# Optimization experiments

Measured on AMD Instinct MI355X. Metric: run time of the kernel, lower is better.

The kernel has to match this reference:

```python
import jax, jax.numpy as jnp
import numpy as np


def setup_inputs() -> dict:
    key = jax.random.key(0)
    k = jax.random.split(key, 5)
    B, S, D, H = 4, 2048, 2048, 8192
    scale1 = 1.0 / np.sqrt(D)
    scale2 = 1.0 / np.sqrt(H)
    return {
        "x": jax.random.normal(k[0], (B, S, D), dtype=jnp.float32),
        "w1": jax.random.normal(k[1], (H, D), dtype=jnp.float32) * scale1,
        "b1": jax.random.normal(k[2], (H,), dtype=jnp.float32) * scale1,
        "w2": jax.random.normal(k[3], (D, H), dtype=jnp.float32) * scale2,
        "b2": jax.random.normal(k[4], (D,), dtype=jnp.float32) * scale2,
    }


def reference(x, w1, b1, w2, b2):
    # fc1: [B,S,D] @ [D,H] -> [B,S,H]
    h = jnp.einsum("bsd,hd->bsh", x, w1) + b1
    # squared ReLU activation
    a = jnp.square(jax.nn.relu(h))
    # fc2: [B,S,H] @ [H,D] -> [B,S,D]
    return jnp.einsum("bsh,dh->bsd", a, w2) + b2
```

## Files before the change

### kernel.cpp

```cpp
#include <hip/hip_runtime.h>
#include <hip/hip_bf16.h>
#include <stdint.h>

typedef __bf16 bf16x8 __attribute__((ext_vector_type(8)));
typedef float f32x4 __attribute__((ext_vector_type(4)));


__device__ inline void gload_lds16(const void* g, void* lds) {
  __builtin_amdgcn_global_load_lds(
      (const __attribute__((address_space(1))) uint32_t*)(uintptr_t)g,
      (__attribute__((address_space(3))) uint32_t*)(uintptr_t)lds,
      16, 0, 0);
}

__device__ inline bf16x8 ds_readv(uint32_t addr) {
  bf16x8 r;
  asm volatile("ds_read_b128 %0, %1" : "=v"(r) : "v"(addr));
  return r;
}

#define LGKM(N) do {                                             \
    asm volatile("s_waitcnt lgkmcnt(" #N ")" ::: "memory");      \
    __builtin_amdgcn_sched_barrier(0);                           \
  } while (0)
#define VM(N) do {                                               \
    asm volatile("s_waitcnt vmcnt(" #N ")" ::: "memory");        \
    __builtin_amdgcn_sched_barrier(0);                           \
  } while (0)

__device__ inline short f2bf(float f) {
  union { float f; uint32_t u; } x; x.f = f;
  uint32_t u = x.u;
  u += 0x7fffu + ((u >> 16) & 1u);
  return (short)(u >> 16);
}

#define BAR() do { asm volatile("" ::: "memory"); \
                   __builtin_amdgcn_s_barrier();  \
                   asm volatile("" ::: "memory"); } while (0)


__global__ __launch_bounds__(256) void cvt_f32_bf16(
    const float* __restrict__ in, short* __restrict__ out, int n4) {
  int i = blockIdx.x * 256 + threadIdx.x;
  if (i < n4) {
    float4 v = reinterpret_cast<const float4*>(in)[i];
    short4 o;
    o.x = f2bf(v.x); o.y = f2bf(v.y); o.z = f2bf(v.z); o.w = f2bf(v.w);
    reinterpret_cast<short4*>(out)[i] = o;
  }
}


template <int EPI>
__global__ __launch_bounds__(512, 2) void gemm_bt(
    const short* __restrict__ A, const short* __restrict__ B,
    const float* __restrict__ bias, void* __restrict__ Cout,
    int M, int N, int K) {
  __shared__ __align__(16) short lds[2][4][128 * 64];

  const int tid  = threadIdx.x;
  const int wave = tid >> 6;
  const int lane = tid & 63;
  const int wr = wave >> 2;
  const int wc = wave & 3;
  const int fr = lane & 15, kq = lane >> 4;

  const int nwg = gridDim.x;
  const int w = (blockIdx.x & 7) * (nwg >> 3) + (blockIdx.x >> 3);
  const int gy = M >> 8;
  const int brow = w % gy;
  const int bcol = w / gy;

  f32x4 acc[8][4];
#pragma unroll
  for (int m = 0; m < 8; ++m)
#pragma unroll
    for (int n = 0; n < 4; ++n)
      acc[m][n] = (f32x4){0.f, 0.f, 0.f, 0.f};

  const int nk = K >> 6;

  const uint32_t LB = (uint32_t)(uintptr_t)&lds[0][0][0];
  uint32_t aA[4][2], aB[2][2];
#pragma unroll
  for (int m = 0; m < 4; ++m)
#pragma unroll
    for (int kk = 0; kk < 2; ++kk) {
      int r = wr * 64 + m * 16 + fr;
      int g = r * 8 + kk * 4 + kq;
      aA[m][kk] = LB + (uint32_t)((g ^ (r & 7)) * 16);
    }
#pragma unroll
  for (int n = 0; n < 2; ++n)
#pragma unroll
    for (int kk = 0; kk < 2; ++kk) {
      int r = wc * 32 + n * 16 + fr;
      int g = r * 8 + kk * 4 + kq;
      aB[n][kk] = LB + (uint32_t)((g ^ (r & 7)) * 16);
    }

  const int i0 = tid;
  const int gl0 = i0 ^ ((i0 >> 3) & 7);
  const int r0 = gl0 >> 3, c0 = gl0 & 7;
  const size_t rstep = (size_t)128 * K;

  const short* pA[2];
  const short* pB[2];
  {
    const int rb0 = (r0 >> 5) * 64 + (r0 & 31);
#pragma unroll
    for (int h = 0; h < 2; ++h) {
      pA[h] = A + (size_t)(brow * 256 + h * 64 + r0) * K + c0 * 8;
      pB[h] = B + (size_t)(bcol * 256 + rb0 + h * 32) * K + c0 * 8;
    }
  }

  const int dst0 = wave * 512, dst1 = 4096 + wave * 512;

#define STAGE(p, buf, slot)                              \
  do {                                                   \
    short* base_ = &lds[buf][slot][0];                   \
    gload_lds16((p), base_ + dst0);                      \
    gload_lds16((p) + rstep, base_ + dst1);              \
    (p) += 64;                                           \
  } while (0)

  bf16x8 a0q[4][2], a1q[4][2], bq0[2][2], bq1[2][2];
  auto Q1 = [&]() {
#pragma unroll
    for (int m = 0; m < 4; ++m)
#pragma unroll
      for (int n = 0; n < 2; ++n)
#pragma unroll
        for (int kk = 0; kk < 2; ++kk)
          acc[m][n] = __builtin_amdgcn_mfma_f32_16x16x32_bf16(
              bq0[n][kk], a0q[m][kk], acc[m][n], 0, 0, 0);
  };
  auto Q2 = [&]() {
#pragma unroll
    for (int m = 0; m < 4; ++m)
#pragma unroll
      for (int n = 0; n < 2; ++n)
#pragma unroll
        for (int kk = 0; kk < 2; ++kk)
          acc[m][n + 2] = __builtin_amdgcn_mfma_f32_16x16x32_bf16(
              bq1[n][kk], a0q[m][kk], acc[m][n + 2], 0, 0, 0);
  };
  auto Q3 = [&]() {
#pragma unroll
    for (int m = 0; m < 4; ++m)
#pragma unroll
      for (int n = 0; n < 2; ++n)
#pragma unroll
        for (int kk = 0; kk < 2; ++kk)
          acc[m + 4][n + 2] = __builtin_amdgcn_mfma_f32_16x16x32_bf16(
              bq1[n][kk], a1q[m][kk], acc[m + 4][n + 2], 0, 0, 0);
  };
  auto Q4 = [&]() {
#pragma unroll
    for (int m = 0; m < 4; ++m)
#pragma unroll
      for (int n = 0; n < 2; ++n)
#pragma unroll
        for (int kk = 0; kk < 2; ++kk)
          acc[m + 4][n] = __builtin_amdgcn_mfma_f32_16x16x32_bf16(
              bq0[n][kk], a1q[m][kk], acc[m + 4][n], 0, 0, 0);
  };
  auto RD_A0 = [&](uint32_t cb) {
#pragma unroll
    for (int m = 0; m < 4; ++m)
#pragma unroll
      for (int kk = 0; kk < 2; ++kk)
        a0q[m][kk] = ds_readv(aA[m][kk] + cb);
  };
  auto RD_A1 = [&](uint32_t cb) {
#pragma unroll
    for (int m = 0; m < 4; ++m)
#pragma unroll
      for (int kk = 0; kk < 2; ++kk)
        a1q[m][kk] = ds_readv(aA[m][kk] + cb + 16384u);
  };
  auto RD_B0 = [&](uint32_t cb) {
#pragma unroll
    for (int n = 0; n < 2; ++n)
#pragma unroll
      for (int kk = 0; kk < 2; ++kk)
        bq0[n][kk] = ds_readv(aB[n][kk] + cb + 32768u);
  };
  auto RD_B1 = [&](uint32_t cb) {
#pragma unroll
    for (int n = 0; n < 2; ++n)
#pragma unroll
      for (int kk = 0; kk < 2; ++kk)
        bq1[n][kk] = ds_readv(aB[n][kk] + cb + 49152u);
  };

#define PRIO_ON  __builtin_amdgcn_s_setprio(1)
#define PRIO_OFF __builtin_amdgcn_s_setprio(0)

  STAGE(pA[0], 0, 0);
  STAGE(pB[0], 0, 2);
  STAGE(pB[1], 0, 3);
  STAGE(pA[1], 0, 1);
  STAGE(pA[0], 1, 0);
  STAGE(pB[0], 1, 2);
  STAGE(pB[1], 1, 3);
  VM(6);
  BAR();

  const int niter = nk >> 1;
  for (int i = 0; i < niter - 1; ++i) {
    RD_A0(0); RD_B0(0);
    STAGE(pA[1], 1, 1);
    LGKM(8);
    BAR();
    LGKM(0);
    PRIO_ON; Q1(); PRIO_OFF;
    VM(10); BAR();
    RD_B1(0);
    STAGE(pA[0], 0, 0);
    BAR();
    LGKM(0);
    PRIO_ON; Q2(); PRIO_OFF;
    VM(10); BAR();
    RD_A1(0);
    STAGE(pB[0], 0, 2);
    BAR();
    LGKM(0);
    PRIO_ON; Q3(); PRIO_OFF;
    VM(10); BAR();
    STAGE(pB[1], 0, 3);
    BAR();
    PRIO_ON; Q4(); PRIO_OFF;
    VM(10); BAR();

    RD_A0(65536u); RD_B0(65536u);
    STAGE(pA[1], 0, 1);
    LGKM(8);
    BAR();
    LGKM(0);
    PRIO_ON; Q1(); PRIO_OFF;
    VM(10); BAR();
    RD_B1(65536u);
    STAGE(pA[0], 1, 0);
    BAR();
    LGKM(0);
    PRIO_ON; Q2(); PRIO_OFF;
    VM(10); BAR();
    RD_A1(65536u);
    STAGE(pB[0], 1, 2);
    BAR();
    LGKM(0);
    PRIO_ON; Q3(); PRIO_OFF;
    VM(10); BAR();
    STAGE(pB[1], 1, 3);
    BAR();
    PRIO_ON; Q4(); PRIO_OFF;
    VM(10); BAR();
  }

  RD_A0(0); RD_B0(0);
  STAGE(pA[1], 1, 1);
  LGKM(8);
  BAR();
  LGKM(0);
  PRIO_ON; Q1(); PRIO_OFF;
  VM(0); BAR();
  RD_B1(0); BAR(); LGKM(0);
  PRIO_ON; Q2(); PRIO_OFF; BAR();
  RD_A1(0); BAR(); LGKM(0);
  PRIO_ON; Q3(); PRIO_OFF; BAR();
  PRIO_ON; Q4(); PRIO_OFF;
  BAR();
  RD_A0(65536u); RD_B0(65536u); BAR(); LGKM(0);
  PRIO_ON; Q1(); PRIO_OFF; BAR();
  RD_B1(65536u); BAR(); LGKM(0);
  PRIO_ON; Q2(); PRIO_OFF; BAR();
  RD_A1(65536u); BAR(); LGKM(0);
  PRIO_ON; Q3(); PRIO_OFF; BAR();
  PRIO_ON; Q4(); PRIO_OFF;

  const int q = lane >> 4;
  if (EPI == 0) {
    short* C = (short*)Cout;
#pragma unroll
    for (int m = 0; m < 8; ++m) {
      const int row = brow * 256 + wr * 128 + m * 16 + fr;
#pragma unroll
      for (int n = 0; n < 4; ++n) {
        const int col = bcol * 256 + wc * 64 + n * 16 + q * 4;
        const float4 bv = *(const float4*)&bias[col];
        short4 o;
        float v0 = acc[m][n][0] + bv.x; v0 = v0 > 0.f ? v0 * v0 : 0.f;
        float v1 = acc[m][n][1] + bv.y; v1 = v1 > 0.f ? v1 * v1 : 0.f;
        float v2 = acc[m][n][2] + bv.z; v2 = v2 > 0.f ? v2 * v2 : 0.f;
        float v3 = acc[m][n][3] + bv.w; v3 = v3 > 0.f ? v3 * v3 : 0.f;
        o.x = f2bf(v0); o.y = f2bf(v1); o.z = f2bf(v2); o.w = f2bf(v3);
        *(short4*)&C[(size_t)row * N + col] = o;
      }
    }
  } else {
    float* C = (float*)Cout;
#pragma unroll
    for (int m = 0; m < 8; ++m) {
      const int row = brow * 256 + wr * 128 + m * 16 + fr;
#pragma unroll
      for (int n = 0; n < 4; ++n) {
        const int col = bcol * 256 + wc * 64 + n * 16 + q * 4;
        const float4 bv = *(const float4*)&bias[col];
        float4 o;
        o.x = acc[m][n][0] + bv.x;
        o.y = acc[m][n][1] + bv.y;
        o.z = acc[m][n][2] + bv.z;
        o.w = acc[m][n][3] + bv.w;
        *(float4*)&C[(size_t)row * N + col] = o;
      }
    }
  }
#undef STAGE
}


extern "C" void kernel_launch(void* const* d_in, const int* in_sizes, int n_in,
                              void* d_out, int out_size, void* d_ws,
                              size_t ws_size, hipStream_t stream) {
  const float* x  = (const float*)d_in[0];
  const float* w1 = (const float*)d_in[1];
  const float* b1 = (const float*)d_in[2];
  const float* w2 = (const float*)d_in[3];
  const float* b2 = (const float*)d_in[4];
  float* out = (float*)d_out;

  const int H = in_sizes[2];
  const int D = in_sizes[4];
  const int M = in_sizes[0] / D;

  short* xb  = (short*)d_ws;
  short* w1b = xb  + (size_t)M * D;
  short* w2b = w1b + (size_t)H * D;
  short* act = w2b + (size_t)D * H;

  {
    int n4 = (M * D) / 4;
    cvt_f32_bf16<<<(n4 + 255) / 256, 256, 0, stream>>>(x, xb, n4);
    n4 = (H * D) / 4;
    cvt_f32_bf16<<<(n4 + 255) / 256, 256, 0, stream>>>(w1, w1b, n4);
    n4 = (D * H) / 4;
    cvt_f32_bf16<<<(n4 + 255) / 256, 256, 0, stream>>>(w2, w2b, n4);
  }

  gemm_bt<0><<<(M / 256) * (H / 256), 512, 0, stream>>>(
      xb, w1b, b1, (void*)act, M, H, D);
  gemm_bt<1><<<(M / 256) * (D / 256), 512, 0, stream>>>(
      act, w2b, b2, (void*)out, M, D, H);
}
```

Measured before the change: 544.4 us.

## Restructure GEMM main loop to halve barriers and overlap staging with MFMA

Reorders the per-quarter schedule in the double-buffered GEMM loop. Each global-to-LDS stage is issued right after a barrier, before its MFMA quarter rather than after it. Two barrier-plus-vmcnt waits per quarter become one, with looser vmcnt thresholds. The aim is to cut synchronisation stalls and overlap global loads with compute. The risk is LDS read/write hazards if the reduced barriers no longer protect buffer reuse.

```diff
diff --git a/kernel.cpp b/kernel.cpp
--- a/kernel.cpp
+++ b/kernel.cpp
@@ -212,73 +212,69 @@
   const int niter = nk >> 1;
   for (int i = 0; i < niter - 1; ++i) {
     RD_A0(0); RD_B0(0);
+    LGKM(8); VM(8);
+    BAR(); LGKM(0);
     STAGE(pA[1], 1, 1);
-    LGKM(8);
+    PRIO_ON; Q1(); PRIO_OFF;
+    RD_B1(0);
+    VM(8);
+    BAR(); LGKM(0);
+    STAGE(pA[0], 0, 0);
+    PRIO_ON; Q2(); PRIO_OFF;
+    RD_A1(0);
+    BAR(); LGKM(0);
+    STAGE(pB[0], 0, 2);
+    PRIO_ON; Q3(); PRIO_OFF;
+    VM(8);
     BAR();
-    LGKM(0);
+    STAGE(pB[1], 0, 3);
+    PRIO_ON; Q4(); PRIO_OFF;
+
+    RD_A0(65536u); RD_B0(65536u);
+    LGKM(8); VM(8);
+    BAR(); LGKM(0);
+    STAGE(pA[1], 0, 1);
     PRIO_ON; Q1(); PRIO_OFF;
-    VM(10); BAR();
-    RD_B1(0);
-    STAGE(pA[0], 0, 0);
+    RD_B1(65536u);
+    VM(8);
+    BAR(); LGKM(0);
+    STAGE(pA[0], 1, 0);
+    PRIO_ON; Q2(); PRIO_OFF;
+    RD_A1(65536u);
+    BAR(); LGKM(0);
+    STAGE(pB[0], 1, 2);
+    PRIO_ON; Q3(); PRIO_OFF;
+    VM(8);
     BAR();
-    LGKM(0);
-    PRIO_ON; Q2(); PRIO_OFF;
-    VM(10); BAR();
-    RD_A1(0);
-    STAGE(pB[0], 0, 2);
-    BAR();
-    LGKM(0);
-    PRIO_ON; Q3(); PRIO_OFF;
-    VM(10); BAR();
-    STAGE(pB[1], 0, 3);
-    BAR();
+    STAGE(pB[1], 1, 3);
     PRIO_ON; Q4(); PRIO_OFF;
-    VM(10); BAR();
-
-    RD_A0(65536u); RD_B0(65536u);
-    STAGE(pA[1], 0, 1);
-    LGKM(8);
-    BAR();
-    LGKM(0);
-    PRIO_ON; Q1(); PRIO_OFF;
-    VM(10); BAR();
-    RD_B1(65536u);
-    STAGE(pA[0], 1, 0);
-    BAR();
-    LGKM(0);
-    PRIO_ON; Q2(); PRIO_OFF;
-    VM(10); BAR();
-    RD_A1(65536u);
-    STAGE(pB[0], 1, 2);
-    BAR();
-    LGKM(0);
-    PRIO_ON; Q3(); PRIO_OFF;
-    VM(10); BAR();
-    STAGE(pB[1], 1, 3);
-    BAR();
-    PRIO_ON; Q4(); PRIO_OFF;
-    VM(10); BAR();
   }
 
   RD_A0(0); RD_B0(0);
+  LGKM(8); VM(0);
+  BAR(); LGKM(0);
   STAGE(pA[1], 1, 1);
+  PRIO_ON; Q1(); PRIO_OFF;
+  RD_B1(0);
+  VM(0);
+  BAR(); LGKM(0);
+  PRIO_ON; Q2(); PRIO_OFF;
+  RD_A1(0);
+  BAR(); LGKM(0);
+  PRIO_ON; Q3(); PRIO_OFF;
+  BAR();
+  PRIO_ON; Q4(); PRIO_OFF;
+
+  RD_A0(65536u); RD_B0(65536u);
   LGKM(8);
-  BAR();
-  LGKM(0);
+  BAR(); LGKM(0);
   PRIO_ON; Q1(); PRIO_OFF;
-  VM(0); BAR();
-  RD_B1(0); BAR(); LGKM(0);
-  PRIO_ON; Q2(); PRIO_OFF; BAR();
-  RD_A1(0); BAR(); LGKM(0);
-  PRIO_ON; Q3(); PRIO_OFF; BAR();
-  PRIO_ON; Q4(); PRIO_OFF;
-  BAR();
-  RD_A0(65536u); RD_B0(65536u); BAR(); LGKM(0);
-  PRIO_ON; Q1(); PRIO_OFF; BAR();
-  RD_B1(65536u); BAR(); LGKM(0);
-  PRIO_ON; Q2(); PRIO_OFF; BAR();
-  RD_A1(65536u); BAR(); LGKM(0);
-  PRIO_ON; Q3(); PRIO_OFF; BAR();
+  RD_B1(65536u);
+  BAR(); LGKM(0);
+  PRIO_ON; Q2(); PRIO_OFF;
+  RD_A1(65536u);
+  BAR(); LGKM(0);
+  PRIO_ON; Q3(); PRIO_OFF;
   PRIO_ON; Q4(); PRIO_OFF;
 
   const int q = lane >> 4;
```

Result: no change. 546.3 us (+0.4%).
